# Optimization experiments

Measured on AMD Instinct MI355X. Metric: run time of the kernel, lower is better.

## Reference

```python
import jax, jax.numpy as jnp
import numpy as np

N_ACT = 300000
C = 128
K = 9
BATCH, H, W = 4, 1024, 1024
EPS = 1e-4  # scn BatchNormalization default eps


def _build_rulebook(rng):
    # sample N_ACT unique active sites on a (BATCH, H, W) grid
    flat = np.sort(rng.choice(BATCH * H * W, size=N_ACT, replace=False).astype(np.int64))
    b = flat // (H * W)
    y = (flat // W) % H
    x = flat % W
    nbr = np.full((N_ACT, K), -1, dtype=np.int32)
    k = 0
    for dy in (-1, 0, 1):
        for dx in (-1, 0, 1):
            ny, nx = y + dy, x + dx
            valid = (ny >= 0) & (ny < H) & (nx >= 0) & (nx < W)
            nflat = b * (H * W) + ny * W + nx
            pos = np.searchsorted(flat, nflat)
            pos_c = np.clip(pos, 0, N_ACT - 1)
            found = valid & (flat[pos_c] == nflat)
            nbr[:, k] = np.where(found, pos_c, -1).astype(np.int32)
            k += 1
    return jnp.asarray(nbr)


def setup_inputs() -> dict:
    key = jax.random.key(0)
    k1, k2, k3 = jax.random.split(key, 3)
    rng = np.random.default_rng(0)
    nbr_idx = _build_rulebook(rng)
    scale = 1.0 / np.sqrt(K * C)
    return {
        "x": jax.random.normal(k1, (N_ACT, C), dtype=jnp.float32),
        "nbr_idx": nbr_idx,
        "W1": jax.random.normal(k2, (K, C, C), dtype=jnp.float32) * scale,
        "gamma1": jnp.ones((C,), jnp.float32),
        "beta1": jnp.zeros((C,), jnp.float32),
        "W2": jax.random.normal(k3, (K, C, C), dtype=jnp.float32) * scale,
        "gamma2": jnp.ones((C,), jnp.float32),
        "beta2": jnp.zeros((C,), jnp.float32),
    }


def _subm_conv(feats, nbr_idx, Wk):
    # gather -> GEMM -> accumulate, one pass per kernel offset (K=9 fixed)
    out = jnp.zeros((feats.shape[0], Wk.shape[2]), feats.dtype)
    for k in range(Wk.shape[0]):
        idx = nbr_idx[:, k]
        mask = (idx >= 0)[:, None]
        g = jnp.where(mask, feats[jnp.maximum(idx, 0)], 0.0)
        out = out + g @ Wk[k]
    return out


def _batchnorm(feats, gamma, beta):
    mean = feats.mean(axis=0)
    var = feats.var(axis=0)  # biased, as in torch BN normalization
    return (feats - mean) * jax.lax.rsqrt(var + EPS) * gamma + beta


def reference(x, nbr_idx, W1, gamma1, beta1, W2, gamma2, beta2):
    out = _subm_conv(x, nbr_idx, W1)
    out = jax.nn.relu(_batchnorm(out, gamma1, beta1))  # BatchNormReLU
    out = _subm_conv(out, nbr_idx, W2)
    out = _batchnorm(out, gamma2, beta2)  # BatchNormalization
    return jax.nn.relu(out + x)  # AddTable + ReLU
```

## Files before the change

kernel.cpp:

```cpp
#include <hip/hip_runtime.h>


#define N_ACT 300000
#define NTAP  9
#define EPSV  1e-4f

using f16x8 = __attribute__((ext_vector_type(8))) _Float16;
using f32x4 = __attribute__((ext_vector_type(4))) float;

#define OFF_T1    0UL
#define OFF_T2    76800000UL
#define OFF_W1    153600000UL
#define OFF_W2    (OFF_W1 + 294912UL)
#define OFF_STATS (OFF_W2 + 294912UL)
#define OFF_SB1H  (OFF_STATS + 2048UL)
#define OFF_SB2   (OFF_SB1H + 512UL)

__device__ __forceinline__ unsigned short f2h(float v) {
  _Float16 h = (_Float16)v;
  return __builtin_bit_cast(unsigned short, h);
}
__device__ __forceinline__ float h2f(unsigned short u) {
  return (float)__builtin_bit_cast(_Float16, u);
}

__global__ void prep_kernel(const float* __restrict__ W1, const float* __restrict__ W2,
                            unsigned short* __restrict__ w1, unsigned short* __restrict__ w2,
                            float* __restrict__ zstats) {
  int b = blockIdx.x, t = threadIdx.x;
  if (b == 36) {
    for (int i = t; i < 512; i += 256) zstats[i] = 0.f;
    return;
  }
  int w = b / 18, rem = b % 18;
  int tap = rem >> 1, ch = rem & 1;
  const float* W = w ? W2 : W1;
  unsigned short* o = w ? w2 : w1;
  int n  = t >> 1;
  int s0 = (t & 1) * 4;
  for (int s = s0; s < s0 + 4; ++s) {
    int sigma = s ^ (n & 7);
    for (int j = 0; j < 8; ++j) {
      int   k = ch * 64 + sigma * 8 + j;
      o[rem * 8192 + n * 64 + s * 8 + j] = f2h(W[tap * 16384 + k * 128 + n]);
    }
  }
}

template <int MODE>
__global__ __launch_bounds__(256, 3)
void conv_kernel(const void* __restrict__ srcv, const int* __restrict__ nbr,
                 const unsigned short* __restrict__ wH,
                 const unsigned short* __restrict__ sbh,
                 unsigned short* __restrict__ outp,
                 float* __restrict__ ssum, float* __restrict__ ssq) {
  __shared__ char smem[32768];
  const int t  = threadIdx.x;
  const int wv = t >> 6, ln = t & 63;
  const int m0 = blockIdx.x * 128;
  const int rs = ln >> 3, sg = ln & 7;
  const int lane16 = ln & 15, g = ln >> 4;
  const int sigma8 = (sg ^ rs) * 8;

  const f16x8 zero8 = {0, 0, 0, 0, 0, 0, 0, 0};

  f16x8 scv0 = zero8, scv1 = zero8, bsv0 = zero8, bsv1 = zero8;
  if (MODE == 1) {
    scv0 = *(const f16x8*)(sbh + sigma8);
    scv1 = *(const f16x8*)(sbh + 64 + sigma8);
    bsv0 = *(const f16x8*)(sbh + 128 + sigma8);
    bsv1 = *(const f16x8*)(sbh + 192 + sigma8);
  }

  f32x4 acc[16];
#pragma unroll
  for (int i = 0; i < 16; ++i) acc[i] = f32x4{0.f, 0.f, 0.f, 0.f};

  for (int tap = 0; tap < NTAP; ++tap) {
    int idx4[4];
#pragma unroll
    for (int it = 0; it < 4; ++it) {
      int gm = m0 + wv * 32 + it * 8 + rs;
      idx4[it] = (gm < N_ACT) ? nbr[gm * 9 + tap] : -1;
    }
#pragma unroll
    for (int ch = 0; ch < 2; ++ch) {
      __syncthreads();
#pragma unroll
      for (int it = 0; it < 4; ++it) {
        int r   = wv * 32 + it * 8 + rs;
        int idx = idx4[it];
        long safe = (long)(idx < 0 ? 0 : idx);
        f16x8 y;
        if (MODE == 0) {
          const float* s = (const float*)srcv + safe * 128 + ch * 64 + sigma8;
          float4 a = *(const float4*)s;
          float4 b = *(const float4*)(s + 4);
          y[0] = (_Float16)a.x; y[1] = (_Float16)a.y; y[2] = (_Float16)a.z; y[3] = (_Float16)a.w;
          y[4] = (_Float16)b.x; y[5] = (_Float16)b.y; y[6] = (_Float16)b.z; y[7] = (_Float16)b.w;
        } else {
          const unsigned short* s = (const unsigned short*)srcv + safe * 128 + ch * 64 + sigma8;
          f16x8 v  = *(const f16x8*)s;
          f16x8 sc = ch ? scv1 : scv0;
          f16x8 bs = ch ? bsv1 : bsv0;
#pragma unroll
          for (int j = 0; j < 8; ++j) {
            _Float16 z = v[j] * sc[j] + bs[j];
            y[j] = z > (_Float16)0 ? z : (_Float16)0;
          }
        }
        if (idx < 0) y = zero8;
        *(f16x8*)(smem + r * 128 + sg * 16) = y;
      }
      {
        const char* gb = (const char*)wH + (tap * 2 + ch) * 16384;
#pragma unroll
        for (int it = 0; it < 4; ++it) {
          int o = wv * 4096 + it * 1024 + ln * 16;
          __builtin_amdgcn_global_load_lds((const __attribute__((address_space(1))) void*)(gb + o),
                                           (__attribute__((address_space(3))) void*)(smem + 16384 + o), 16, 0, 0);
        }
      }
      __syncthreads();
#pragma unroll
      for (int ks = 0; ks < 2; ++ks) {
        f16x8 ah[4], bh[4];
        int sigma = ks * 4 + g;
#pragma unroll
        for (int mt = 0; mt < 4; ++mt) {
          int m = (wv & 1) * 64 + mt * 16 + lane16;
          ah[mt] = *(const f16x8*)(smem + m * 128 + ((sigma ^ (m & 7)) * 16));
        }
#pragma unroll
        for (int nt = 0; nt < 4; ++nt) {
          int n = (wv >> 1) * 64 + nt * 16 + lane16;
          bh[nt] = *(const f16x8*)(smem + 16384 + n * 128 + ((sigma ^ (n & 7)) * 16));
        }
#pragma unroll
        for (int mt = 0; mt < 4; ++mt)
#pragma unroll
          for (int nt = 0; nt < 4; ++nt)
            acc[mt * 4 + nt] = __builtin_amdgcn_mfma_f32_16x16x32_f16(ah[mt], bh[nt], acc[mt * 4 + nt], 0, 0, 0);
      }
    }
  }
  int rowbase = m0 + (wv & 1) * 64;
  int colbase = (wv >> 1) * 64;
  float s[4], q[4];
#pragma unroll
  for (int nt = 0; nt < 4; ++nt) { s[nt] = 0.f; q[nt] = 0.f; }
#pragma unroll
  for (int mt = 0; mt < 4; ++mt)
#pragma unroll
    for (int nt = 0; nt < 4; ++nt)
#pragma unroll
      for (int r = 0; r < 4; ++r) {
        float v  = acc[mt * 4 + nt][r];
        int  row = rowbase + mt * 16 + g * 4 + r;
        int  col = colbase + nt * 16 + lane16;
        if (row < N_ACT) outp[row * 128 + col] = f2h(v);
        s[nt] += v; q[nt] += v * v;
      }
  __syncthreads();
  float* sbuf = (float*)smem;
  float* qbuf = ((float*)smem) + 256;
#pragma unroll
  for (int nt = 0; nt < 4; ++nt) {
    float sv = s[nt], qv = q[nt];
    sv += __shfl_xor(sv, 16, 64); sv += __shfl_xor(sv, 32, 64);
    qv += __shfl_xor(qv, 16, 64); qv += __shfl_xor(qv, 32, 64);
    if (ln < 16) { sbuf[wv * 64 + nt * 16 + ln] = sv; qbuf[wv * 64 + nt * 16 + ln] = qv; }
  }
  __syncthreads();
  if (t < 128) {
    int c = t;
    float tot = (c < 64) ? (sbuf[c] + sbuf[64 + c]) : (sbuf[128 + (c - 64)] + sbuf[192 + (c - 64)]);
    atomicAdd(ssum + c, tot);
  } else {
    int c = t - 128;
    float tot = (c < 64) ? (qbuf[c] + qbuf[64 + c]) : (qbuf[128 + (c - 64)] + qbuf[192 + (c - 64)]);
    atomicAdd(ssq + c, tot);
  }
}

__global__ void finalize1_kernel(const float* __restrict__ ssum, const float* __restrict__ ssq,
                                 const float* __restrict__ gamma, const float* __restrict__ beta,
                                 unsigned short* __restrict__ sbh) {
  int c = threadIdx.x;
  float mean = ssum[c] * (1.f / N_ACT);
  float var  = ssq[c] * (1.f / N_ACT) - mean * mean;
  float sc   = rsqrtf(var + EPSV) * gamma[c];
  sbh[c]       = f2h(sc);
  sbh[128 + c] = f2h(beta[c] - mean * sc);
}

__global__ void finalize2_kernel(const float* __restrict__ ssum, const float* __restrict__ ssq,
                                 const float* __restrict__ gamma, const float* __restrict__ beta,
                                 float* __restrict__ scale, float* __restrict__ bias) {
  int c = threadIdx.x;
  float mean = ssum[c] * (1.f / N_ACT);
  float var  = ssq[c] * (1.f / N_ACT) - mean * mean;
  float sc   = rsqrtf(var + EPSV) * gamma[c];
  scale[c] = sc;
  bias[c]  = beta[c] - mean * sc;
}

__global__ void final_kernel(const unsigned short* __restrict__ t2,
                             const float* __restrict__ scale, const float* __restrict__ bias,
                             const float* __restrict__ x, float* __restrict__ outp) {
  int i = (blockIdx.x * 256 + threadIdx.x) * 4;
  int c = i & 127;
  ushort4 hv = *(const ushort4*)(t2 + i);
  float4 sc  = *(const float4*)(scale + c);
  float4 bs  = *(const float4*)(bias + c);
  float4 xx  = *(const float4*)(x + i);
  float4 o;
  o.x = fmaxf(h2f(hv.x) * sc.x + bs.x + xx.x, 0.f);
  o.y = fmaxf(h2f(hv.y) * sc.y + bs.y + xx.y, 0.f);
  o.z = fmaxf(h2f(hv.z) * sc.z + bs.z + xx.z, 0.f);
  o.w = fmaxf(h2f(hv.w) * sc.w + bs.w + xx.w, 0.f);
  *(float4*)(outp + i) = o;
}

extern "C" void kernel_launch(void* const* d_in, const int* in_sizes, int n_in,
                              void* d_out, int out_size, void* d_ws, size_t ws_size,
                              hipStream_t stream) {
  const float* x   = (const float*)d_in[0];
  const int*   nbr = (const int*)d_in[1];
  const float* W1  = (const float*)d_in[2];
  const float* g1  = (const float*)d_in[3];
  const float* b1  = (const float*)d_in[4];
  const float* W2  = (const float*)d_in[5];
  const float* g2  = (const float*)d_in[6];
  const float* b2  = (const float*)d_in[7];
  float* out = (float*)d_out;
  char*  ws  = (char*)d_ws;

  unsigned short* t1  = (unsigned short*)(ws + OFF_T1);
  unsigned short* t2  = (unsigned short*)(ws + OFF_T2);
  unsigned short* w1  = (unsigned short*)(ws + OFF_W1);
  unsigned short* w2  = (unsigned short*)(ws + OFF_W2);
  float*          st  = (float*)(ws + OFF_STATS);
  unsigned short* sbh = (unsigned short*)(ws + OFF_SB1H);
  float*          sc2 = (float*)(ws + OFF_SB2);
  float*          bs2 = sc2 + 128;

  prep_kernel<<<37, 256, 0, stream>>>(W1, W2, w1, w2, st);
  conv_kernel<0><<<2344, 256, 0, stream>>>(x, nbr, w1, nullptr, t1, st, st + 128);
  finalize1_kernel<<<1, 128, 0, stream>>>(st, st + 128, g1, b1, sbh);
  conv_kernel<1><<<2344, 256, 0, stream>>>(t1, nbr, w2, sbh, t2, st + 256, st + 384);
  finalize2_kernel<<<1, 128, 0, stream>>>(st + 256, st + 384, g2, b2, sc2, bs2);
  final_kernel<<<37500, 256, 0, stream>>>(t2, sc2, bs2, x, out);
}
```

Baseline: 626.1 us.

## Gather conv inputs via direct global-to-LDS loads with fp16 pre-conversion

Adds a pass that converts x to fp16 up front, so both convolutions can gather neighbor rows straight into LDS with global_load_lds instead of going through registers. Missing neighbors are pointed at a special row: zeros for the first conv, and the value -bias/scale for the second, so that after BN+ReLU they come out as zero. The BN+ReLU of the second conv moves from the gather stage to the MFMA operand reads. Occupancy is raised to 4 blocks per SM. The cost is an extra conversion kernel and its memory traffic, repeated BN math on A fragments, and possible fp16 rounding error in the -bias/scale trick.

```diff
diff --git a/kernel.cpp b/kernel.cpp
--- a/kernel.cpp
+++ b/kernel.cpp
@@ -8,13 +8,16 @@
 using f16x8 = __attribute__((ext_vector_type(8))) _Float16;
 using f32x4 = __attribute__((ext_vector_type(4))) float;
 
-#define OFF_T1    0UL
-#define OFF_T2    76800000UL
-#define OFF_W1    153600000UL
+#define OFF_PH    0UL
+#define OFF_T1    76800000UL
+#define OFF_T2    153600000UL
+#define OFF_W1    230400000UL
 #define OFF_W2    (OFF_W1 + 294912UL)
 #define OFF_STATS (OFF_W2 + 294912UL)
 #define OFF_SB1H  (OFF_STATS + 2048UL)
-#define OFF_SB2   (OFF_SB1H + 512UL)
+#define OFF_ZB0   (OFF_SB1H + 512UL)
+#define OFF_ZB1   (OFF_ZB0 + 256UL)
+#define OFF_SB2   (OFF_ZB1 + 256UL)
 
 __device__ __forceinline__ unsigned short f2h(float v) {
   _Float16 h = (_Float16)v;
@@ -26,10 +29,11 @@
 
 __global__ void prep_kernel(const float* __restrict__ W1, const float* __restrict__ W2,
                             unsigned short* __restrict__ w1, unsigned short* __restrict__ w2,
-                            float* __restrict__ zstats) {
+                            float* __restrict__ zstats, float* __restrict__ zrow0) {
   int b = blockIdx.x, t = threadIdx.x;
   if (b == 36) {
     for (int i = t; i < 512; i += 256) zstats[i] = 0.f;
+    if (t < 64) zrow0[t] = 0.f;
     return;
   }
   int w = b / 18, rem = b % 18;
@@ -41,17 +45,30 @@
   for (int s = s0; s < s0 + 4; ++s) {
     int sigma = s ^ (n & 7);
     for (int j = 0; j < 8; ++j) {
-      int   k = ch * 64 + sigma * 8 + j;
+      int k = ch * 64 + sigma * 8 + j;
       o[rem * 8192 + n * 64 + s * 8 + j] = f2h(W[tap * 16384 + k * 128 + n]);
     }
   }
 }
 
+__global__ void tohalf_kernel(const float* __restrict__ x, unsigned short* __restrict__ ph) {
+  int i = (blockIdx.x * 256 + threadIdx.x) * 8;
+  float4 a = *(const float4*)(x + i);
+  float4 b = *(const float4*)(x + i + 4);
+  uint4 p;
+  p.x = (unsigned)f2h(a.x) | ((unsigned)f2h(a.y) << 16);
+  p.y = (unsigned)f2h(a.z) | ((unsigned)f2h(a.w) << 16);
+  p.z = (unsigned)f2h(b.x) | ((unsigned)f2h(b.y) << 16);
+  p.w = (unsigned)f2h(b.z) | ((unsigned)f2h(b.w) << 16);
+  *(uint4*)(ph + i) = p;
+}
+
 template <int MODE>
-__global__ __launch_bounds__(256, 3)
-void conv_kernel(const void* __restrict__ srcv, const int* __restrict__ nbr,
+__global__ __launch_bounds__(256, 4)
+void conv_kernel(const unsigned short* __restrict__ pH, const int* __restrict__ nbr,
                  const unsigned short* __restrict__ wH,
                  const unsigned short* __restrict__ sbh,
+                 const unsigned short* __restrict__ zrow,
                  unsigned short* __restrict__ outp,
                  float* __restrict__ ssum, float* __restrict__ ssq) {
   __shared__ char smem[32768];
@@ -62,14 +79,16 @@
   const int lane16 = ln & 15, g = ln >> 4;
   const int sigma8 = (sg ^ rs) * 8;
 
-  const f16x8 zero8 = {0, 0, 0, 0, 0, 0, 0, 0};
-
-  f16x8 scv0 = zero8, scv1 = zero8, bsv0 = zero8, bsv1 = zero8;
+  f16x8 scv[2][2], bsv[2][2];
   if (MODE == 1) {
-    scv0 = *(const f16x8*)(sbh + sigma8);
-    scv1 = *(const f16x8*)(sbh + 64 + sigma8);
-    bsv0 = *(const f16x8*)(sbh + 128 + sigma8);
-    bsv1 = *(const f16x8*)(sbh + 192 + sigma8);
+#pragma unroll
+    for (int ch = 0; ch < 2; ++ch)
+#pragma unroll
+      for (int ks = 0; ks < 2; ++ks) {
+        int c = ch * 64 + (ks * 4 + g) * 8;
+        scv[ch][ks] = *(const f16x8*)(sbh + c);
+        bsv[ch][ks] = *(const f16x8*)(sbh + 128 + c);
+      }
   }
 
   f32x4 acc[16];
@@ -90,27 +109,10 @@
       for (int it = 0; it < 4; ++it) {
         int r   = wv * 32 + it * 8 + rs;
         int idx = idx4[it];
-        long safe = (long)(idx < 0 ? 0 : idx);
-        f16x8 y;
-        if (MODE == 0) {
-          const float* s = (const float*)srcv + safe * 128 + ch * 64 + sigma8;
-          float4 a = *(const float4*)s;
-          float4 b = *(const float4*)(s + 4);
-          y[0] = (_Float16)a.x; y[1] = (_Float16)a.y; y[2] = (_Float16)a.z; y[3] = (_Float16)a.w;
-          y[4] = (_Float16)b.x; y[5] = (_Float16)b.y; y[6] = (_Float16)b.z; y[7] = (_Float16)b.w;
-        } else {
-          const unsigned short* s = (const unsigned short*)srcv + safe * 128 + ch * 64 + sigma8;
-          f16x8 v  = *(const f16x8*)s;
-          f16x8 sc = ch ? scv1 : scv0;
-          f16x8 bs = ch ? bsv1 : bsv0;
-#pragma unroll
-          for (int j = 0; j < 8; ++j) {
-            _Float16 z = v[j] * sc[j] + bs[j];
-            y[j] = z > (_Float16)0 ? z : (_Float16)0;
-          }
-        }
-        if (idx < 0) y = zero8;
-        *(f16x8*)(smem + r * 128 + sg * 16) = y;
+        long off = (long)(idx < 0 ? 0 : idx) * 128 + ch * 64 + sigma8;
+        const unsigned short* gs = (idx >= 0) ? (pH + off) : (zrow + ch * 64 + sigma8);
+        __builtin_amdgcn_global_load_lds((const __attribute__((address_space(1))) void*)gs,
+                                         (__attribute__((address_space(3))) void*)(smem + r * 128 + sg * 16), 16, 0, 0);
       }
       {
         const char* gb = (const char*)wH + (tap * 2 + ch) * 16384;
@@ -130,6 +132,16 @@
         for (int mt = 0; mt < 4; ++mt) {
           int m = (wv & 1) * 64 + mt * 16 + lane16;
           ah[mt] = *(const f16x8*)(smem + m * 128 + ((sigma ^ (m & 7)) * 16));
+        }
+        if (MODE == 1) {
+          f16x8 sc = scv[ch][ks], bs = bsv[ch][ks];
+#pragma unroll
+          for (int mt = 0; mt < 4; ++mt)
+#pragma unroll
+            for (int j = 0; j < 8; ++j) {
+              _Float16 z = ah[mt][j] * sc[j] + bs[j];
+              ah[mt][j] = z > (_Float16)0 ? z : (_Float16)0;
+            }
         }
 #pragma unroll
         for (int nt = 0; nt < 4; ++nt) {
@@ -185,13 +197,17 @@
 
 __global__ void finalize1_kernel(const float* __restrict__ ssum, const float* __restrict__ ssq,
                                  const float* __restrict__ gamma, const float* __restrict__ beta,
-                                 unsigned short* __restrict__ sbh) {
+                                 unsigned short* __restrict__ sbh, unsigned short* __restrict__ zrow1) {
   int c = threadIdx.x;
   float mean = ssum[c] * (1.f / N_ACT);
   float var  = ssq[c] * (1.f / N_ACT) - mean * mean;
   float sc   = rsqrtf(var + EPSV) * gamma[c];
+  float bs   = beta[c] - mean * sc;
   sbh[c]       = f2h(sc);
-  sbh[128 + c] = f2h(beta[c] - mean * sc);
+  sbh[128 + c] = f2h(bs);
+  float hs = h2f(f2h(sc)), hb = h2f(f2h(bs));
+  float z  = (hs != 0.f) ? (-hb / hs) : 0.f;
+  zrow1[c] = f2h(z);
 }
 
 __global__ void finalize2_kernel(const float* __restrict__ ssum, const float* __restrict__ ssq,
@@ -236,19 +252,23 @@
   float* out = (float*)d_out;
   char*  ws  = (char*)d_ws;
 
+  unsigned short* ph  = (unsigned short*)(ws + OFF_PH);
   unsigned short* t1  = (unsigned short*)(ws + OFF_T1);
   unsigned short* t2  = (unsigned short*)(ws + OFF_T2);
   unsigned short* w1  = (unsigned short*)(ws + OFF_W1);
   unsigned short* w2  = (unsigned short*)(ws + OFF_W2);
   float*          st  = (float*)(ws + OFF_STATS);
   unsigned short* sbh = (unsigned short*)(ws + OFF_SB1H);
+  unsigned short* zb0 = (unsigned short*)(ws + OFF_ZB0);
+  unsigned short* zb1 = (unsigned short*)(ws + OFF_ZB1);
   float*          sc2 = (float*)(ws + OFF_SB2);
   float*          bs2 = sc2 + 128;
 
-  prep_kernel<<<37, 256, 0, stream>>>(W1, W2, w1, w2, st);
-  conv_kernel<0><<<2344, 256, 0, stream>>>(x, nbr, w1, nullptr, t1, st, st + 128);
-  finalize1_kernel<<<1, 128, 0, stream>>>(st, st + 128, g1, b1, sbh);
-  conv_kernel<1><<<2344, 256, 0, stream>>>(t1, nbr, w2, sbh, t2, st + 256, st + 384);
+  prep_kernel<<<37, 256, 0, stream>>>(W1, W2, w1, w2, st, (float*)zb0);
+  tohalf_kernel<<<18750, 256, 0, stream>>>(x, ph);
+  conv_kernel<0><<<2344, 256, 0, stream>>>(ph, nbr, w1, nullptr, zb0, t1, st, st + 128);
+  finalize1_kernel<<<1, 128, 0, stream>>>(st, st + 128, g1, b1, sbh, zb1);
+  conv_kernel<1><<<2344, 256, 0, stream>>>(t1, nbr, w2, sbh, zb1, t2, st + 256, st + 384);
   finalize2_kernel<<<1, 128, 0, stream>>>(st + 256, st + 384, g2, b2, sc2, bs2);
   final_kernel<<<37500, 256, 0, stream>>>(t2, sc2, bs2, x, out);
 }
```

Measured after the change: 812.5 us. +29.8%, slower.
